# Kernel tuning notes

Measured on AMD Instinct MI355X. Metric: run time of the kernel, lower is better.

The kernel has to match this reference:

```python
import jax, jax.numpy as jnp
import numpy as np

# SSD prior config (small VGGLite-style)
FEATURE_MAPS = [10, 5, 3, 1]
BOXES_PER_LOC = [4, 4, 4, 4]
IMG = 128      # ssd_config.DATA.SHAPE[0] -> WhereTransformer image_size
OBJ = 64
ZWHAT = 64
HID = 512
B = 4
N_OBJ = sum(f * f for f in FEATURE_MAPS)                       # 135
N_FEAT = sum(b * f * f for f, b in zip(FEATURE_MAPS, BOXES_PER_LOC))  # 540


def reconstruction_indices():
    # Replicates Decoder.reconstruction_indices: map per-location latents to per-box slots.
    idx = []
    last = 0
    for f, bpl in zip(FEATURE_MAPS, BOXES_PER_LOC):
        for i in range(f * f):
            idx.extend([last + i] * bpl)
        last += f * f
    return np.asarray(idx, dtype=np.int32)


def what_decode(z, W1, b1, W2, b2):
    # WhatDecoder: MLP z_what -> 3xOBJxOBJ object glyph in (0,1)
    h = jax.nn.relu(z @ W1 + b1)
    return jax.nn.sigmoid(h @ W2 + b2).reshape(-1, 3, OBJ, OBJ)


def where_stn(imgs, zw):
    # WhereTransformer: paste each object image into its (cx, cy, w, h) box on an IMGxIMG canvas
    # via inverse-affine bilinear sampling with zero padding (STN / grid_sample semantics).
    cx, cy, w, h = zw[:, 0], zw[:, 1], zw[:, 2], zw[:, 3]
    w = jnp.maximum(w, 1e-2)
    h = jnp.maximum(h, 1e-2)
    lin = jnp.linspace(-1.0, 1.0, IMG)
    gy, gx = jnp.meshgrid(lin, lin, indexing='ij')           # (IMG, IMG)
    u = (gx[None] - (2.0 * cx - 1.0)[:, None, None]) / w[:, None, None]
    v = (gy[None] - (2.0 * cy - 1.0)[:, None, None]) / h[:, None, None]
    px = (u + 1.0) * 0.5 * (OBJ - 1)                          # (N, IMG, IMG)
    py = (v + 1.0) * 0.5 * (OBJ - 1)

    def sample_one(img, py, px):  # img: (3, OBJ, OBJ)
        x0 = jnp.floor(px); y0 = jnp.floor(py)
        wx = px - x0; wy = py - y0
        x0i = x0.astype(jnp.int32); y0i = y0.astype(jnp.int32)

        def tap(yi, xi, wgt):
            valid = (yi >= 0) & (yi < OBJ) & (xi >= 0) & (xi < OBJ)
            yc = jnp.clip(yi, 0, OBJ - 1)
            xc = jnp.clip(xi, 0, OBJ - 1)
            return img[:, yc, xc] * (wgt * valid)[None]

        return (tap(y0i, x0i, (1 - wy) * (1 - wx)) + tap(y0i, x0i + 1, (1 - wy) * wx)
                + tap(y0i + 1, x0i, wy * (1 - wx)) + tap(y0i + 1, x0i + 1, wy * wx))

    return jax.vmap(sample_one)(imgs, py, px)                 # (N, 3, IMG, IMG)


def setup_inputs() -> dict:
    key = jax.random.key(0)
    ks = jax.random.split(key, 8)
    return {
        'z_what': jax.random.normal(ks[0], (B, N_OBJ, ZWHAT), jnp.float32),
        'z_where': jax.random.uniform(ks[1], (B, N_FEAT, 4), jnp.float32),
        'z_depth': jax.random.normal(ks[2], (B, N_OBJ, 1), jnp.float32),
        'W1': jax.random.normal(ks[3], (ZWHAT, HID), jnp.float32) * 0.05,
        'b1': jnp.zeros((HID,), jnp.float32),
        'W2': jax.random.normal(ks[4], (HID, 3 * OBJ * OBJ), jnp.float32) * 0.02,
        'b2': jnp.zeros((3 * OBJ * OBJ,), jnp.float32),
        'z_present': jax.random.randint(ks[5], (B, N_FEAT, 1), 0, 2, jnp.int32),
    }


def reference(z_what, z_where, z_depth, W1, b1, W2, b2, z_present):
    idx = jnp.asarray(reconstruction_indices())
    # index_select: replicate per-location latents across boxes-per-location
    zw_full = z_what[:, idx]                                  # (B, N_FEAT, ZWHAT)
    zd_full = z_depth[:, idx]                                 # (B, N_FEAT, 1)
    # sort descending by depth; gather all latents in that order
    order = jnp.argsort(-zd_full[..., 0], axis=1)             # (B, N_FEAT)
    s_what = jnp.take_along_axis(zw_full, order[..., None], axis=1)
    s_where = jnp.take_along_axis(z_where, order[..., None], axis=1)
    s_pres = jnp.take_along_axis(z_present, order[..., None], axis=1)
    # decode + STN warp all objects; absent objects are zeroed (equivalent to the
    dec = what_decode(s_what.reshape(-1, ZWHAT), W1, b1, W2, b2)
    warped = where_stn(dec, s_where.reshape(-1, 4))
    imgs = warped.reshape(B, N_FEAT, 3, IMG, IMG) * s_pres.astype(warped.dtype)[..., None, None]
    # depth compositing: per channel-pixel, take the first nonzero value in sorted order
    nz = imgs != 0
    first = jnp.argmax(nz, axis=1)                            # (B, 3, IMG, IMG)
    out = jnp.take_along_axis(imgs, first[:, None], axis=1)[:, 0] * nz.any(axis=1)
    return out
```

## Files before the change

kernel.cpp:

```cpp
#include <hip/hip_runtime.h>
#include <hip/hip_bf16.h>
#include <math.h>

#define NBOX  540
#define NOBJ  135
#define ZW    64
#define HIDN  512
#define NOUT  12288
#define OBJS  64
#define BATCH 4
#define MROWS 540
#define MPAD  640

#define PRE_SORT   4
#define PRE_GEMM1  MPAD
#define PRE_CVT    ((NOUT / 64) * (HIDN / 64))
#define PRE_BLOCKS (PRE_SORT + PRE_GEMM1 + PRE_CVT)

#define OFF_N      0u
#define OFF_PARAMS 256u
#define OFF_OBJS   34816u
#define OFF_HBF    43520u
#define OFF_W2T    698880u
#define OFF_DEC    13281792u

typedef short  bf16x8 __attribute__((ext_vector_type(8)));
typedef float  f32x4  __attribute__((ext_vector_type(4)));

#define GLOAD_LDS16(gp, lp)                                                    \
  __builtin_amdgcn_global_load_lds(                                            \
      (const __attribute__((address_space(1))) void*)(gp),                     \
      (__attribute__((address_space(3))) void*)(lp), 16, 0, 0)

__device__ __forceinline__ unsigned short f2bf(float x) {
  __hip_bfloat16 h = __float2bfloat16(x);
  return *(unsigned short*)&h;
}

__global__ __launch_bounds__(256) void k_pre(
    const float* __restrict__ z_depth,
    const float* __restrict__ z_where,
    const int*   __restrict__ z_present,
    const float* __restrict__ Z,
    const float* __restrict__ W1,
    const float* __restrict__ b1,
    const float* __restrict__ W2,
    float4* __restrict__ params,
    int*    __restrict__ objs,
    int*    __restrict__ n_present,
    unsigned short* __restrict__ Hbf,
    unsigned short* __restrict__ W2T)
{
  __shared__ unsigned long long keys[256];
  __shared__ int wsums[4], woff[4];
  __shared__ float zs[ZW];
  __shared__ unsigned int T[64 * 36];

  const int bid = blockIdx.x;
  const int t   = threadIdx.x;

  if (bid < PRE_SORT) {
    const int b = bid;
    unsigned long long key = ~0ull;
    if (t < NOBJ) {
      unsigned u = __float_as_uint(z_depth[b * NOBJ + t]);
      u = (u & 0x80000000u) ? ~u : (u | 0x80000000u);
      key = ((unsigned long long)(~u) << 32) | (unsigned)t;
    }
    keys[t] = key;
    __syncthreads();
    for (int k = 2; k <= 256; k <<= 1) {
      for (int j = k >> 1; j > 0; j >>= 1) {
        int ixj = t ^ j;
        if (ixj > t) {
          unsigned long long a = keys[t], c = keys[ixj];
          bool asc = (t & k) == 0;
          if (asc ? (a > c) : (a < c)) { keys[t] = c; keys[ixj] = a; }
        }
        __syncthreads();
      }
    }
    int boxq[3]; int presq[3]; int cnt = 0;
#pragma unroll
    for (int q = 0; q < 3; q++) {
      int e = 3 * t + q;
      presq[q] = 0; boxq[q] = 0;
      if (e < NBOX) {
        int o  = (int)(keys[e >> 2] & 0xFFFFFFFFull);
        int bx = o * 4 + (e & 3);
        boxq[q]  = bx;
        presq[q] = (z_present[b * NBOX + bx] != 0) ? 1 : 0;
        cnt += presq[q];
      }
    }
    int lane = t & 63, wv = t >> 6;
    int incl = cnt;
#pragma unroll
    for (int o = 1; o < 64; o <<= 1) {
      int vprev = __shfl_up(incl, o, 64);
      if (lane >= o) incl += vprev;
    }
    if (lane == 63) wsums[wv] = incl;
    __syncthreads();
    if (t == 0) {
      int a = 0;
#pragma unroll
      for (int i = 0; i < 4; i++) { woff[i] = a; a += wsums[i]; }
      n_present[b] = a;
    }
    __syncthreads();
    int slot = woff[wv] + incl - cnt;
#pragma unroll
    for (int q = 0; q < 3; q++) {
      if (presq[q]) {
        const float* zw = z_where + ((size_t)b * NBOX + boxq[q]) * 4;
        params[b * NBOX + slot] = make_float4(zw[0], zw[1], zw[2], zw[3]);
        objs[b * NBOX + slot]   = boxq[q] >> 2;
        slot++;
      }
    }
  } else if (bid < PRE_SORT + PRE_GEMM1) {
    const int r = bid - PRE_SORT;
    if (r >= MROWS) {
      Hbf[(size_t)r * HIDN + t] = 0;
      Hbf[(size_t)r * HIDN + t + 256] = 0;
      return;
    }
    if (t < ZW) zs[t] = Z[(size_t)r * ZW + t];
    __syncthreads();
    float a0 = b1[t], a1 = b1[t + 256];
#pragma unroll 8
    for (int k = 0; k < ZW; k++) {
      float z = zs[k];
      a0 += z * W1[(size_t)k * HIDN + t];
      a1 += z * W1[(size_t)k * HIDN + t + 256];
    }
    Hbf[(size_t)r * HIDN + t]       = f2bf(fmaxf(a0, 0.f));
    Hbf[(size_t)r * HIDN + t + 256] = f2bf(fmaxf(a1, 0.f));
  } else {
    const int c  = bid - PRE_SORT - PRE_GEMM1;
    const int n0 = (c % (NOUT / 64)) * 64;
    const int k0 = (c / (NOUT / 64)) * 64;
#pragma unroll
    for (int p = 0; p < 2; p++) {
      int kp = p * 16 + (t >> 4);
      int n4 = t & 15;
      int k  = k0 + kp * 2;
      float4 a = *(const float4*)&W2[(size_t)k * NOUT + n0 + n4 * 4];
      float4 b = *(const float4*)&W2[(size_t)(k + 1) * NOUT + n0 + n4 * 4];
      T[(n4*4 + 0) * 36 + kp] = (unsigned)f2bf(a.x) | ((unsigned)f2bf(b.x) << 16);
      T[(n4*4 + 1) * 36 + kp] = (unsigned)f2bf(a.y) | ((unsigned)f2bf(b.y) << 16);
      T[(n4*4 + 2) * 36 + kp] = (unsigned)f2bf(a.z) | ((unsigned)f2bf(b.z) << 16);
      T[(n4*4 + 3) * 36 + kp] = (unsigned)f2bf(a.w) | ((unsigned)f2bf(b.w) << 16);
    }
    __syncthreads();
#pragma unroll
    for (int p = 0; p < 2; p++) {
      int cc = p * 256 + t;
      int n = cc >> 3, ch = cc & 7;
      uint4 v = *(const uint4*)&T[n * 36 + ch * 4];
      *(uint4*)&W2T[(size_t)(n0 + n) * HIDN + k0 + ch * 8] = v;
    }
  }
}

__global__ __launch_bounds__(256) void k_gemm2_mfma(
    const unsigned short* __restrict__ Hbf,
    const unsigned short* __restrict__ W2T,
    const float* __restrict__ b2,
    float* __restrict__ dec)
{
  __shared__ unsigned short As[128 * 32];
  __shared__ unsigned short Bs[128 * 32];
  const int t    = threadIdx.x;
  const int lane = t & 63, wv = t >> 6;
  const int n0 = blockIdx.x * 128;
  const int m0 = blockIdx.y * 128;
  const int wm = (wv & 1) * 64, wn = (wv >> 1) * 64;

  const int r0 = t >> 2;
  const int kc0 = (t & 3) ^ (r0 & 3);
  const int r1 = r0 + 64;
  const int kc1 = (t & 3) ^ (r1 & 3);

  const int fr = lane & 15;
  const int fj = lane >> 4;
  f32x4 acc[4][4] = {};

  for (int k0 = 0; k0 < HIDN; k0 += 32) {
    GLOAD_LDS16(Hbf + (size_t)(m0 + r0) * HIDN + k0 + kc0 * 8, &As[t * 8]);
    GLOAD_LDS16(Hbf + (size_t)(m0 + r1) * HIDN + k0 + kc1 * 8, &As[(t + 256) * 8]);
    GLOAD_LDS16(W2T + (size_t)(n0 + r0) * HIDN + k0 + kc0 * 8, &Bs[t * 8]);
    GLOAD_LDS16(W2T + (size_t)(n0 + r1) * HIDN + k0 + kc1 * 8, &Bs[(t + 256) * 8]);
    __syncthreads();

    bf16x8 av[4], bv[4];
#pragma unroll
    for (int mi = 0; mi < 4; mi++) {
      int row = wm + mi * 16 + fr;
      av[mi] = *(const bf16x8*)&As[(row * 4 + (fj ^ (row & 3))) * 8];
    }
#pragma unroll
    for (int ni = 0; ni < 4; ni++) {
      int row = wn + ni * 16 + fr;
      bv[ni] = *(const bf16x8*)&Bs[(row * 4 + (fj ^ (row & 3))) * 8];
    }
#pragma unroll
    for (int mi = 0; mi < 4; mi++)
#pragma unroll
      for (int ni = 0; ni < 4; ni++)
        acc[mi][ni] = __builtin_amdgcn_mfma_f32_16x16x32_bf16(av[mi], bv[ni], acc[mi][ni], 0, 0, 0);
    __syncthreads();
  }

#pragma unroll
  for (int ni = 0; ni < 4; ni++) {
    int col = n0 + wn + ni * 16 + fr;
    float bb = b2[col];
#pragma unroll
    for (int mi = 0; mi < 4; mi++) {
#pragma unroll
      for (int r = 0; r < 4; r++) {
        int row = m0 + wm + mi * 16 + fj * 4 + r;
        if (row < MROWS) {
          float v = acc[mi][ni][r] + bb;
          dec[(size_t)row * NOUT + col] = 1.0f / (1.0f + __expf(-v));
        }
      }
    }
  }
}

__global__ __launch_bounds__(256) void k_composite(
    const float4* __restrict__ params, const int* __restrict__ objs,
    const int* __restrict__ n_present, const float* __restrict__ dec,
    float* __restrict__ out)
{
#pragma clang fp contract(off)
  __shared__ float4 sp[NBOX];
  __shared__ int sobj[NBOX];
  const int bid  = blockIdx.x;
  const int t    = threadIdx.x;
  const int b    = bid >> 6;
  const int tile = bid & 63;
  const int y = (tile >> 3) * 16 + (t >> 4);
  const int x = (tile & 7) * 16 + (t & 15);
  const int n = n_present[b];
  for (int i = t; i < n; i += 256) {
    sp[i]   = params[b * NBOX + i];
    sobj[i] = objs[b * NBOX + i];
  }
  __syncthreads();

  const double step = 2.0 / 127.0;
  const double gx = (x == 127) ? 1.0 : ((double)x * step + (-1.0));
  const double gy = (y == 127) ? 1.0 : ((double)y * step + (-1.0));

  float o0 = 0.f, o1 = 0.f, o2 = 0.f;
  bool done = false;
  for (int j = 0; j < n; j++) {
    if (__all((int)done)) break;
    if (!done) {
      float4 p = sp[j];
      double w = fmax((double)p.z, 0.01);
      double h = fmax((double)p.w, 0.01);
      double tx = 2.0 * (double)p.x - 1.0;
      double ty = 2.0 * (double)p.y - 1.0;
      double u = (gx - tx) / w;
      double v = (gy - ty) / h;
      double px = (u + 1.0) * 0.5 * 63.0;
      double py = (v + 1.0) * 0.5 * 63.0;
      double fx = floor(px), fy = floor(py);
      double wx = px - fx, wy = py - fy;
      int x0 = (int)fx, y0 = (int)fy;
      int x1 = x0 + 1, y1 = y0 + 1;
      bool vx0 = (x0 >= 0) && (x0 < OBJS);
      bool vx1 = (x1 >= 0) && (x1 < OBJS);
      bool vy0 = (y0 >= 0) && (y0 < OBJS);
      bool vy1 = (y1 >= 0) && (y1 < OBJS);
      double w00 = (1.0 - wy) * (1.0 - wx);
      double w01 = (1.0 - wy) * wx;
      double w10 = wy * (1.0 - wx);
      double w11 = wy * wx;
      bool c00 = vy0 && vx0 && (w00 > 0.0);
      bool c01 = vy0 && vx1 && (w01 > 0.0);
      bool c10 = vy1 && vx0 && (w10 > 0.0);
      bool c11 = vy1 && vx1 && (w11 > 0.0);
      if (c00 | c01 | c10 | c11) {
        const float* g = dec + (size_t)(b * NOBJ + sobj[j]) * NOUT;
        double s0 = 0.0, s1 = 0.0, s2 = 0.0;
        if (c00) { int o = y0*64 + x0; s0 += g[o]*w00; s1 += g[4096+o]*w00; s2 += g[8192+o]*w00; }
        if (c01) { int o = y0*64 + x1; s0 += g[o]*w01; s1 += g[4096+o]*w01; s2 += g[8192+o]*w01; }
        if (c10) { int o = y1*64 + x0; s0 += g[o]*w10; s1 += g[4096+o]*w10; s2 += g[8192+o]*w10; }
        if (c11) { int o = y1*64 + x1; s0 += g[o]*w11; s1 += g[4096+o]*w11; s2 += g[8192+o]*w11; }
        o0 = (float)s0; o1 = (float)s1; o2 = (float)s2;
        done = true;
      }
    }
  }
  const int ob = b * 3 * 16384 + y * 128 + x;
  out[ob]         = o0;
  out[ob + 16384] = o1;
  out[ob + 32768] = o2;
}

extern "C" void kernel_launch(void* const* d_in, const int* in_sizes, int n_in,
                              void* d_out, int out_size, void* d_ws, size_t ws_size,
                              hipStream_t stream) {
  (void)in_sizes; (void)n_in; (void)out_size; (void)ws_size;
  const float* z_what    = (const float*)d_in[0];
  const float* z_where   = (const float*)d_in[1];
  const float* z_depth   = (const float*)d_in[2];
  const float* W1        = (const float*)d_in[3];
  const float* b1        = (const float*)d_in[4];
  const float* W2        = (const float*)d_in[5];
  const float* b2        = (const float*)d_in[6];
  const int*   z_present = (const int*)d_in[7];
  float* out = (float*)d_out;
  char* ws = (char*)d_ws;

  int*            n_present = (int*)(ws + OFF_N);
  float4*         params    = (float4*)(ws + OFF_PARAMS);
  int*            objs      = (int*)(ws + OFF_OBJS);
  unsigned short* Hbf       = (unsigned short*)(ws + OFF_HBF);
  unsigned short* W2T       = (unsigned short*)(ws + OFF_W2T);
  float*          dec       = (float*)(ws + OFF_DEC);

  k_pre<<<dim3(PRE_BLOCKS), dim3(256), 0, stream>>>(
      z_depth, z_where, z_present, z_what, W1, b1, W2,
      params, objs, n_present, Hbf, W2T);
  k_gemm2_mfma<<<dim3(NOUT / 128, MPAD / 128), dim3(256), 0, stream>>>(Hbf, W2T, b2, dec);
  k_composite<<<dim3(256), dim3(256), 0, stream>>>(params, objs, n_present, dec, out);
}
```

Baseline: 140.0 us.

## Fuse W2 bf16 conversion into GEMM2 tile load and store decoder output as bf16

Drops the separate pass that converts and transposes W2 to bf16. The GEMM2 kernel now reads fp32 W2 directly, converts it in registers and writes it into the swizzled LDS tile. The depth sort moves into extra blocks of the GEMM2 launch, and GEMM1 becomes its own kernel. Decoder output is stored as bf16 to halve the traffic of writing dec and gathering from it in compositing, at the cost of precision and of W2 being reread by each of the five M-tiles through synchronous loads instead of async global-to-LDS copies.

```diff
diff --git a/kernel.cpp b/kernel.cpp
--- a/kernel.cpp
+++ b/kernel.cpp
@@ -12,17 +12,14 @@
 #define MROWS 540
 #define MPAD  640
 
-#define PRE_SORT   4
-#define PRE_GEMM1  MPAD
-#define PRE_CVT    ((NOUT / 64) * (HIDN / 64))
-#define PRE_BLOCKS (PRE_SORT + PRE_GEMM1 + PRE_CVT)
+#define G2_TILES ((NOUT / 128) * (MPAD / 128))
+#define G2_BLOCKS (G2_TILES + BATCH)
 
 #define OFF_N      0u
 #define OFF_PARAMS 256u
 #define OFF_OBJS   34816u
 #define OFF_HBF    43520u
-#define OFF_W2T    698880u
-#define OFF_DEC    13281792u
+#define OFF_DEC    698880u
 
 typedef short  bf16x8 __attribute__((ext_vector_type(8)));
 typedef float  f32x4  __attribute__((ext_vector_type(4)));
@@ -36,31 +33,56 @@
   __hip_bfloat16 h = __float2bfloat16(x);
   return *(unsigned short*)&h;
 }
-
-__global__ __launch_bounds__(256) void k_pre(
+__device__ __forceinline__ float bf2f(unsigned short u) {
+  return __uint_as_float((unsigned)u << 16);
+}
+
+__global__ __launch_bounds__(256) void k_gemm1(
+    const float* __restrict__ Z, const float* __restrict__ W1,
+    const float* __restrict__ b1, unsigned short* __restrict__ Hbf)
+{
+  __shared__ float zs[ZW];
+  const int r = blockIdx.x;
+  const int t = threadIdx.x;
+  if (r >= MROWS) {
+    Hbf[(size_t)r * HIDN + t] = 0;
+    Hbf[(size_t)r * HIDN + t + 256] = 0;
+    return;
+  }
+  if (t < ZW) zs[t] = Z[(size_t)r * ZW + t];
+  __syncthreads();
+  float a0 = b1[t], a1 = b1[t + 256];
+#pragma unroll 8
+  for (int k = 0; k < ZW; k++) {
+    float z = zs[k];
+    a0 += z * W1[(size_t)k * HIDN + t];
+    a1 += z * W1[(size_t)k * HIDN + t + 256];
+  }
+  Hbf[(size_t)r * HIDN + t]       = f2bf(fmaxf(a0, 0.f));
+  Hbf[(size_t)r * HIDN + t + 256] = f2bf(fmaxf(a1, 0.f));
+}
+
+__global__ __launch_bounds__(256) void k_gemm2_mfma(
+    const unsigned short* __restrict__ Hbf,
+    const float* __restrict__ W2,
+    const float* __restrict__ b2,
+    unsigned short* __restrict__ dec,
     const float* __restrict__ z_depth,
     const float* __restrict__ z_where,
     const int*   __restrict__ z_present,
-    const float* __restrict__ Z,
-    const float* __restrict__ W1,
-    const float* __restrict__ b1,
-    const float* __restrict__ W2,
     float4* __restrict__ params,
     int*    __restrict__ objs,
-    int*    __restrict__ n_present,
-    unsigned short* __restrict__ Hbf,
-    unsigned short* __restrict__ W2T)
+    int*    __restrict__ n_present)
 {
-  __shared__ unsigned long long keys[256];
+  __shared__ unsigned short As[128 * 32];
+  __shared__ unsigned short Bs[128 * 32];
   __shared__ int wsums[4], woff[4];
-  __shared__ float zs[ZW];
-  __shared__ unsigned int T[64 * 36];
-
   const int bid = blockIdx.x;
   const int t   = threadIdx.x;
 
-  if (bid < PRE_SORT) {
-    const int b = bid;
+  if (bid >= G2_TILES) {
+    const int b = bid - G2_TILES;
+    unsigned long long* keys = (unsigned long long*)As;
     unsigned long long key = ~0ull;
     if (t < NOBJ) {
       unsigned u = __float_as_uint(z_depth[b * NOBJ + t]);
@@ -119,63 +141,12 @@
         slot++;
       }
     }
-  } else if (bid < PRE_SORT + PRE_GEMM1) {
-    const int r = bid - PRE_SORT;
-    if (r >= MROWS) {
-      Hbf[(size_t)r * HIDN + t] = 0;
-      Hbf[(size_t)r * HIDN + t + 256] = 0;
-      return;
-    }
-    if (t < ZW) zs[t] = Z[(size_t)r * ZW + t];
-    __syncthreads();
-    float a0 = b1[t], a1 = b1[t + 256];
-#pragma unroll 8
-    for (int k = 0; k < ZW; k++) {
-      float z = zs[k];
-      a0 += z * W1[(size_t)k * HIDN + t];
-      a1 += z * W1[(size_t)k * HIDN + t + 256];
-    }
-    Hbf[(size_t)r * HIDN + t]       = f2bf(fmaxf(a0, 0.f));
-    Hbf[(size_t)r * HIDN + t + 256] = f2bf(fmaxf(a1, 0.f));
-  } else {
-    const int c  = bid - PRE_SORT - PRE_GEMM1;
-    const int n0 = (c % (NOUT / 64)) * 64;
-    const int k0 = (c / (NOUT / 64)) * 64;
-#pragma unroll
-    for (int p = 0; p < 2; p++) {
-      int kp = p * 16 + (t >> 4);
-      int n4 = t & 15;
-      int k  = k0 + kp * 2;
-      float4 a = *(const float4*)&W2[(size_t)k * NOUT + n0 + n4 * 4];
-      float4 b = *(const float4*)&W2[(size_t)(k + 1) * NOUT + n0 + n4 * 4];
-      T[(n4*4 + 0) * 36 + kp] = (unsigned)f2bf(a.x) | ((unsigned)f2bf(b.x) << 16);
-      T[(n4*4 + 1) * 36 + kp] = (unsigned)f2bf(a.y) | ((unsigned)f2bf(b.y) << 16);
-      T[(n4*4 + 2) * 36 + kp] = (unsigned)f2bf(a.z) | ((unsigned)f2bf(b.z) << 16);
-      T[(n4*4 + 3) * 36 + kp] = (unsigned)f2bf(a.w) | ((unsigned)f2bf(b.w) << 16);
-    }
-    __syncthreads();
-#pragma unroll
-    for (int p = 0; p < 2; p++) {
-      int cc = p * 256 + t;
-      int n = cc >> 3, ch = cc & 7;
-      uint4 v = *(const uint4*)&T[n * 36 + ch * 4];
-      *(uint4*)&W2T[(size_t)(n0 + n) * HIDN + k0 + ch * 8] = v;
-    }
-  }
-}
-
-__global__ __launch_bounds__(256) void k_gemm2_mfma(
-    const unsigned short* __restrict__ Hbf,
-    const unsigned short* __restrict__ W2T,
-    const float* __restrict__ b2,
-    float* __restrict__ dec)
-{
-  __shared__ unsigned short As[128 * 32];
-  __shared__ unsigned short Bs[128 * 32];
-  const int t    = threadIdx.x;
+    return;
+  }
+
   const int lane = t & 63, wv = t >> 6;
-  const int n0 = blockIdx.x * 128;
-  const int m0 = blockIdx.y * 128;
+  const int n0 = (bid % (NOUT / 128)) * 128;
+  const int m0 = (bid / (NOUT / 128)) * 128;
   const int wm = (wv & 1) * 64, wn = (wv >> 1) * 64;
 
   const int r0 = t >> 2;
@@ -183,6 +154,9 @@
   const int r1 = r0 + 64;
   const int kc1 = (t & 3) ^ (r1 & 3);
 
+  const int bn  = t & 127;
+  const int bkh = t >> 7;
+
   const int fr = lane & 15;
   const int fj = lane >> 4;
   f32x4 acc[4][4] = {};
@@ -190,8 +164,21 @@
   for (int k0 = 0; k0 < HIDN; k0 += 32) {
     GLOAD_LDS16(Hbf + (size_t)(m0 + r0) * HIDN + k0 + kc0 * 8, &As[t * 8]);
     GLOAD_LDS16(Hbf + (size_t)(m0 + r1) * HIDN + k0 + kc1 * 8, &As[(t + 256) * 8]);
-    GLOAD_LDS16(W2T + (size_t)(n0 + r0) * HIDN + k0 + kc0 * 8, &Bs[t * 8]);
-    GLOAD_LDS16(W2T + (size_t)(n0 + r1) * HIDN + k0 + kc1 * 8, &Bs[(t + 256) * 8]);
+
+    float v[16];
+    const float* wp = W2 + (size_t)(k0 + bkh * 16) * NOUT + n0 + bn;
+#pragma unroll
+    for (int i = 0; i < 16; i++) v[i] = wp[(size_t)i * NOUT];
+#pragma unroll
+    for (int c2 = 0; c2 < 2; c2++) {
+      int cix = bkh * 2 + c2;
+      unsigned pk[4];
+#pragma unroll
+      for (int j = 0; j < 4; j++)
+        pk[j] = (unsigned)f2bf(v[c2 * 8 + 2 * j]) |
+                ((unsigned)f2bf(v[c2 * 8 + 2 * j + 1]) << 16);
+      *(uint4*)&Bs[(bn * 4 + (cix ^ (bn & 3))) * 8] = make_uint4(pk[0], pk[1], pk[2], pk[3]);
+    }
     __syncthreads();
 
     bf16x8 av[4], bv[4];
@@ -223,8 +210,8 @@
       for (int r = 0; r < 4; r++) {
         int row = m0 + wm + mi * 16 + fj * 4 + r;
         if (row < MROWS) {
-          float v = acc[mi][ni][r] + bb;
-          dec[(size_t)row * NOUT + col] = 1.0f / (1.0f + __expf(-v));
+          float vpre = acc[mi][ni][r] + bb;
+          dec[(size_t)row * NOUT + col] = f2bf(1.0f / (1.0f + __expf(-vpre)));
         }
       }
     }
@@ -233,7 +220,7 @@
 
 __global__ __launch_bounds__(256) void k_composite(
     const float4* __restrict__ params, const int* __restrict__ objs,
-    const int* __restrict__ n_present, const float* __restrict__ dec,
+    const int* __restrict__ n_present, const unsigned short* __restrict__ dec,
     float* __restrict__ out)
 {
 #pragma clang fp contract(off)
@@ -287,12 +274,12 @@
       bool c10 = vy1 && vx0 && (w10 > 0.0);
       bool c11 = vy1 && vx1 && (w11 > 0.0);
       if (c00 | c01 | c10 | c11) {
-        const float* g = dec + (size_t)(b * NOBJ + sobj[j]) * NOUT;
+        const unsigned short* g = dec + (size_t)(b * NOBJ + sobj[j]) * NOUT;
         double s0 = 0.0, s1 = 0.0, s2 = 0.0;
-        if (c00) { int o = y0*64 + x0; s0 += g[o]*w00; s1 += g[4096+o]*w00; s2 += g[8192+o]*w00; }
-        if (c01) { int o = y0*64 + x1; s0 += g[o]*w01; s1 += g[4096+o]*w01; s2 += g[8192+o]*w01; }
-        if (c10) { int o = y1*64 + x0; s0 += g[o]*w10; s1 += g[4096+o]*w10; s2 += g[8192+o]*w10; }
-        if (c11) { int o = y1*64 + x1; s0 += g[o]*w11; s1 += g[4096+o]*w11; s2 += g[8192+o]*w11; }
+        if (c00) { int o = y0*64 + x0; s0 += bf2f(g[o])*w00; s1 += bf2f(g[4096+o])*w00; s2 += bf2f(g[8192+o])*w00; }
+        if (c01) { int o = y0*64 + x1; s0 += bf2f(g[o])*w01; s1 += bf2f(g[4096+o])*w01; s2 += bf2f(g[8192+o])*w01; }
+        if (c10) { int o = y1*64 + x0; s0 += bf2f(g[o])*w10; s1 += bf2f(g[4096+o])*w10; s2 += bf2f(g[8192+o])*w10; }
+        if (c11) { int o = y1*64 + x1; s0 += bf2f(g[o])*w11; s1 += bf2f(g[4096+o])*w11; s2 += bf2f(g[8192+o])*w11; }
         o0 = (float)s0; o1 = (float)s1; o2 = (float)s2;
         done = true;
       }
@@ -323,12 +310,10 @@
   float4*         params    = (float4*)(ws + OFF_PARAMS);
   int*            objs      = (int*)(ws + OFF_OBJS);
   unsigned short* Hbf       = (unsigned short*)(ws + OFF_HBF);
-  unsigned short* W2T       = (unsigned short*)(ws + OFF_W2T);
-  float*          dec       = (float*)(ws + OFF_DEC);
-
-  k_pre<<<dim3(PRE_BLOCKS), dim3(256), 0, stream>>>(
-      z_depth, z_where, z_present, z_what, W1, b1, W2,
-      params, objs, n_present, Hbf, W2T);
-  k_gemm2_mfma<<<dim3(NOUT / 128, MPAD / 128), dim3(256), 0, stream>>>(Hbf, W2T, b2, dec);
+  unsigned short* dec       = (unsigned short*)(ws + OFF_DEC);
+
+  k_gemm1<<<dim3(MPAD), dim3(256), 0, stream>>>(z_what, W1, b1, Hbf);
+  k_gemm2_mfma<<<dim3(G2_BLOCKS), dim3(256), 0, stream>>>(
+      Hbf, W2, b2, dec, z_depth, z_where, z_present, params, objs, n_present);
   k_composite<<<dim3(256), dim3(256), 0, stream>>>(params, objs, n_present, dec, out);
 }
```

Measured after the change: 140.4 us. No clear change (+0.3%).
